# Kernel tuning notes

Measured on AMD Instinct MI355X. Metric: run time of the kernel, lower is better.

## Reference

```python
import jax, jax.numpy as jnp
import numpy as np

D_IN, H, V = 512, 1024, 32000
S, B, T = 64, 128, 48
MARGIN = 0.1


def setup_inputs() -> dict:
    key = jax.random.key(0)
    ks = jax.random.split(key, 16)
    sc = 0.05
    f = lambda k, shp: jax.random.normal(k, shp, jnp.float32) * sc
    emb_W = f(ks[0], (V, D_IN)).at[0].set(0.0)  # padding_idx=0 row is zero
    return dict(
        ctx=jax.random.normal(ks[1], (S, B, H), jnp.float32),
        ctx_mask=jnp.ones((S, B), jnp.float32),
        y=jax.random.randint(ks[2], (T, B), 0, V),
        emb_W=emb_W,
        W_init=f(ks[3], (H, H)), b_init=jnp.zeros((H,), jnp.float32),
        W_ih0=f(ks[4], (3 * H, D_IN)), W_hh0=f(ks[5], (3 * H, H)),
        b_ih0=jnp.zeros((3 * H,), jnp.float32), b_hh0=jnp.zeros((3 * H,), jnp.float32),
        W_c2c=f(ks[6], (H, H)), W_h2c=f(ks[7], (H, H)), v_att=f(ks[8], (H,)),
        W_ih1=f(ks[9], (3 * H, H)), W_hh1=f(ks[10], (3 * H, H)),
        b_ih1=jnp.zeros((3 * H,), jnp.float32), b_hh1=jnp.zeros((3 * H,), jnp.float32),
        W_h2o=f(ks[11], (D_IN, H)), b_h2o=jnp.zeros((D_IN,), jnp.float32),
        W_out=f(ks[12], (V, D_IN)),
    )


def _gru(x, h, Wih, Whh, bih, bhh):
    # torch.nn.GRUCell math
    gi = x @ Wih.T + bih
    gh = h @ Whh.T + bhh
    ir, iz, inn = jnp.split(gi, 3, axis=-1)
    hr, hz, hn = jnp.split(gh, 3, axis=-1)
    r = jax.nn.sigmoid(ir + hr)
    z = jax.nn.sigmoid(iz + hz)
    n = jnp.tanh(inn + r * hn)
    return (1.0 - z) * n + z * h


def reference(ctx, ctx_mask, y, emb_W, W_init, b_init, W_ih0, W_hh0, b_ih0, b_hh0,
              W_c2c, W_h2c, v_att, W_ih1, W_hh1, b_ih1, b_hh1, W_h2o, b_h2o, W_out):
    # dec_init='mean_ctx': tanh(FF(masked mean over source))
    mean_ctx = ctx.sum(0) / ctx_mask.sum(0)[:, None]            # (B,H)
    h = jnp.tanh(mean_ctx @ W_init.T + b_init)                  # h0 (B,H)

    ctx_p = jnp.einsum('sbc,dc->sbd', ctx, W_c2c)               # ctx2ctx, hoisted out of loop
    neg = jnp.where(ctx_mask > 0, 0.0, -1e9)                    # (S,B) additive mask
    W_out_n = W_out / jnp.linalg.norm(W_out, axis=-1, keepdims=True)

    emb_in = emb_W[y[:-1]]                                      # (T-1,B,D_IN)
    targets = y[1:]                                             # (T-1,B)

    def step(h, inp):
        e, tgt = inp
        h1 = _gru(e, h, W_ih0, W_hh0, b_ih0, b_hh0)             # dec0
        # MLP attention: v^T tanh(ctx2ctx(ctx) + hid2ctx(h1))
        scores = jnp.tanh(ctx_p + (h1 @ W_h2c.T)[None]) @ v_att + neg   # (S,B)
        alpha = jax.nn.softmax(scores, axis=0)
        z_t = jnp.einsum('sb,sbc->bc', alpha, ctx)              # context (B,H)
        h2 = _gru(z_t, h1, W_ih1, W_hh1, b_ih1, b_hh1)          # dec1
        logit = jnp.tanh(h2 @ W_h2o.T + b_h2o)                  # hid2out
        logit = logit / jnp.linalg.norm(logit, axis=-1, keepdims=True)
        log_p = logit @ W_out_n.T                               # (B,V) cosine sims
        # max-margin loss, contrastive_type='max', ignore pad (tgt==0)
        s_true = jnp.take_along_axis(log_p, tgt[:, None], axis=1)
        viol = jnp.maximum(MARGIN - s_true + log_p, 0.0)
        viol = viol * (1.0 - jax.nn.one_hot(tgt, V, dtype=log_p.dtype))
        l = jnp.sum(jnp.where(tgt != 0, viol.max(-1), 0.0))
        return h2, l

    _, losses = jax.lax.scan(step, h, (emb_in, targets))
    return losses.sum()
```

## Files before the change

### kernel.cpp

```cpp
#include <hip/hip_runtime.h>
#include <math.h>

#define H    1024
#define H3   3072
#define DIN  512
#define VSZ  32000
#define SS   64
#define BB   128
#define TP   47
#define NROWS (TP*BB)
#define VCHUNKS 250
#define FMARGIN 0.1f
#define NBLK 256
#define HS   65536
#define CTXPL_S 62

typedef unsigned short u16;
typedef unsigned int u32;
typedef unsigned long long u64;
typedef __bf16 bf16_t;
typedef bf16_t bf16x8 __attribute__((ext_vector_type(8)));
typedef float f32x4 __attribute__((ext_vector_type(4)));
typedef u16 u16x4 __attribute__((ext_vector_type(4)));
typedef u16 u16x8 __attribute__((ext_vector_type(8)));

#define MFMA __builtin_amdgcn_mfma_f32_16x16x32_bf16

__device__ inline u16 f2bf(float f){
    unsigned b = __float_as_uint(f);
    return (u16)((b + 0x7FFFu + ((b >> 16) & 1u)) >> 16);
}
__device__ inline float bf2f(u16 u){ return __uint_as_float(((unsigned)u) << 16); }
__device__ inline float sigm(float x){ return 1.f/(1.f + expf(-x)); }

__device__ inline void stoval(float* p, float v){ *p = v; }
__device__ inline void stoval(u16* p, float v){ *p = f2bf(v); }

__device__ inline void cstore(u32* p, u32 v){ __hip_atomic_store(p, v, __ATOMIC_RELAXED, __HIP_MEMORY_SCOPE_AGENT); }
__device__ inline void cstoref(float* p, float v){ __hip_atomic_store(p, v, __ATOMIC_RELAXED, __HIP_MEMORY_SCOPE_AGENT); }
__device__ inline void cstore64(u64* p, u64 v){ __hip_atomic_store(p, v, __ATOMIC_RELAXED, __HIP_MEMORY_SCOPE_AGENT); }
__device__ inline float cloadf(const float* p){ return __hip_atomic_load(p, __ATOMIC_RELAXED, __HIP_MEMORY_SCOPE_AGENT); }

__device__ inline void gbar(u32* bar, u32* mygen, int tid, int bid){
    __syncthreads();
    if (tid == 0){
        u32 tgt = ++(*mygen);
        __builtin_amdgcn_s_waitcnt(0);
        u32* cnt = bar + 64 + (bid >> 3)*32;
        u32 old = __hip_atomic_fetch_add(cnt, 1u, __ATOMIC_RELAXED, __HIP_MEMORY_SCOPE_AGENT);
        if (old == 7u){
            __hip_atomic_store(cnt, 0u, __ATOMIC_RELAXED, __HIP_MEMORY_SCOPE_AGENT);
            u32 old2 = __hip_atomic_fetch_add(&bar[1], 1u, __ATOMIC_RELEASE, __HIP_MEMORY_SCOPE_AGENT);
            if (old2 == 31u){
                __hip_atomic_store(&bar[1], 0u, __ATOMIC_RELAXED, __HIP_MEMORY_SCOPE_AGENT);
                __hip_atomic_store(&bar[0], tgt, __ATOMIC_RELEASE, __HIP_MEMORY_SCOPE_AGENT);
            }
        }
        while (__hip_atomic_load(&bar[0], __ATOMIC_RELAXED, __HIP_MEMORY_SCOPE_AGENT) < tgt)
            __builtin_amdgcn_s_sleep(1);
    }
    __syncthreads();
    asm volatile("" ::: "memory");
}


__global__ __launch_bounds__(128) void k_mask_sum(const float* __restrict__ mask, float* __restrict__ msum){
    int b = threadIdx.x;
    if (b < BB){ float s = 0.f; for (int i = 0; i < SS; i++) s += mask[i*BB + b]; msum[b] = s; }
}

__global__ __launch_bounds__(256) void k_mean_ctx(const float* __restrict__ ctx, const float* __restrict__ msum,
                                                  float* __restrict__ mean){
    int idx = blockIdx.x*256 + threadIdx.x;
    if (idx < BB*H){
        float s = 0.f;
        for (int i = 0; i < SS; i++) s += ctx[(size_t)i*BB*H + idx];
        mean[idx] = s / msum[idx / H];
    }
}

__global__ __launch_bounds__(256) void k_f32bf(const float* __restrict__ in, u16* __restrict__ out, int n4){
    int i = blockIdx.x*256 + threadIdx.x;
    if (i >= n4) return;
    float4 v = ((const float4*)in)[i];
    u16x4 o = { f2bf(v.x), f2bf(v.y), f2bf(v.z), f2bf(v.w) };
    ((u16x4*)out)[i] = o;
}

__global__ __launch_bounds__(256) void k_pack_h0(const float* __restrict__ h0, u32* __restrict__ hsHI,
                                                 u32* __restrict__ hsLO){
    int i = blockIdx.x*256 + threadIdx.x;
    float v0 = h0[i*2], v1 = h0[i*2 + 1];
    u16 a = f2bf(v0), b = f2bf(v1);
    hsHI[i] = (u32)a | ((u32)b << 16);
    hsLO[i] = (u32)f2bf(v0 - bf2f(a)) | ((u32)f2bf(v1 - bf2f(b)) << 16);
}

__global__ __launch_bounds__(256) void k_f2bf_frag(const float* __restrict__ in, u16* __restrict__ out,
                                                   int RK8, int K8){
    int t = blockIdx.x*256 + threadIdx.x;
    if (t >= RK8) return;
    int r = t / K8, k8 = t - r*K8;
    const float* p = in + (size_t)r*K8*8 + k8*8;
    float4 a = *(const float4*)p;
    float4 b = *(const float4*)(p + 4);
    size_t dst = ((size_t)(r >> 4)*(K8 >> 2) + (k8 >> 2))*512 + (size_t)((r & 15) + (k8 & 3)*16)*8;
    u16x8 o;
    o[0]=f2bf(a.x); o[1]=f2bf(a.y); o[2]=f2bf(a.z); o[3]=f2bf(a.w);
    o[4]=f2bf(b.x); o[5]=f2bf(b.y); o[6]=f2bf(b.z); o[7]=f2bf(b.w);
    *(u16x8*)(out + dst) = o;
}

__global__ __launch_bounds__(256) void k_rownorm_frag(const float* __restrict__ in, u16* __restrict__ out,
                                                      int nrows){
    int w = threadIdx.x >> 6, lane = threadIdx.x & 63;
    int row = blockIdx.x*4 + w;
    if (row >= nrows) return;
    const float* r = in + (size_t)row*512 + lane*8;
    float4 a = *(const float4*)r;
    float4 b = *(const float4*)(r + 4);
    float s = a.x*a.x + a.y*a.y + a.z*a.z + a.w*a.w
            + b.x*b.x + b.y*b.y + b.z*b.z + b.w*b.w;
    #pragma unroll
    for (int off = 32; off; off >>= 1) s += __shfl_xor(s, off);
    float inv = rsqrtf(s);
    size_t dst = ((size_t)(row >> 4)*16 + (lane >> 2))*512 + (size_t)((row & 15) + (lane & 3)*16)*8;
    u16x8 o;
    o[0]=f2bf(a.x*inv); o[1]=f2bf(a.y*inv); o[2]=f2bf(a.z*inv); o[3]=f2bf(a.w*inv);
    o[4]=f2bf(b.x*inv); o[5]=f2bf(b.y*inv); o[6]=f2bf(b.z*inv); o[7]=f2bf(b.w*inv);
    *(u16x8*)(out + dst) = o;
}

__global__ __launch_bounds__(256) void k_emb_frag(const float* __restrict__ emb, const int* __restrict__ y,
                                                  u16* __restrict__ out){
    int w = threadIdx.x >> 6, lane = threadIdx.x & 63;
    int row = blockIdx.x*4 + w;
    int src = y[row];
    const float* r = emb + (size_t)src*512 + lane*8;
    float4 a = *(const float4*)r;
    float4 b = *(const float4*)(r + 4);
    size_t dst = ((size_t)(row >> 4)*16 + (lane >> 2))*512 + (size_t)((row & 15) + (lane & 3)*16)*8;
    u16x8 o;
    o[0]=f2bf(a.x); o[1]=f2bf(a.y); o[2]=f2bf(a.z); o[3]=f2bf(a.w);
    o[4]=f2bf(b.x); o[5]=f2bf(b.y); o[6]=f2bf(b.z); o[7]=f2bf(b.w);
    *(u16x8*)(out + dst) = o;
}

template<int ACT>
__global__ __launch_bounds__(256) void k_gemm_nt(const float* __restrict__ A, const float* __restrict__ W,
                                                 const float* __restrict__ bias, float* __restrict__ C,
                                                 int M, int N, int K){
    __shared__ float As[16][68];
    __shared__ float Ws[16][68];
    int tid = threadIdx.x;
    int bm = blockIdx.y*64, bn = blockIdx.x*64;
    int lr = tid >> 2;
    int lk = (tid & 3) * 4;
    int tr = (tid >> 4) * 4;
    int tc = (tid & 15) * 4;
    float acc[4][4] = {};
    const float* Abase = A + (size_t)(bm + lr)*K;
    const float* Wbase = W + (size_t)(bn + lr)*K;
    for (int k0 = 0; k0 < K; k0 += 16){
        float4 av = *(const float4*)(Abase + k0 + lk);
        float4 wv = *(const float4*)(Wbase + k0 + lk);
        __syncthreads();
        As[lk+0][lr]=av.x; As[lk+1][lr]=av.y; As[lk+2][lr]=av.z; As[lk+3][lr]=av.w;
        Ws[lk+0][lr]=wv.x; Ws[lk+1][lr]=wv.y; Ws[lk+2][lr]=wv.z; Ws[lk+3][lr]=wv.w;
        __syncthreads();
        #pragma unroll
        for (int kk = 0; kk < 16; kk++){
            float4 a = *(const float4*)&As[kk][tr];
            float4 w = *(const float4*)&Ws[kk][tc];
            acc[0][0] += a.x*w.x; acc[0][1] += a.x*w.y; acc[0][2] += a.x*w.z; acc[0][3] += a.x*w.w;
            acc[1][0] += a.y*w.x; acc[1][1] += a.y*w.y; acc[1][2] += a.y*w.z; acc[1][3] += a.y*w.w;
            acc[2][0] += a.z*w.x; acc[2][1] += a.z*w.y; acc[2][2] += a.z*w.z; acc[2][3] += a.z*w.w;
            acc[3][0] += a.w*w.x; acc[3][1] += a.w*w.y; acc[3][2] += a.w*w.z; acc[3][3] += a.w*w.w;
        }
    }
    #pragma unroll
    for (int i = 0; i < 4; i++){
        #pragma unroll
        for (int j = 0; j < 4; j++){
            float v = acc[i][j];
            if (bias) v += bias[bn + tc + j];
            if (ACT == 1) v = tanhf(v);
            C[(size_t)(bm + tr + i)*N + bn + tc + j] = v;
        }
    }
}

template<int AFRAG, int ACT, typename OutT>
__global__ __launch_bounds__(256) void k_gemmf(const u16* __restrict__ A, const u16* __restrict__ B,
                                               const float* __restrict__ bias, OutT* __restrict__ C,
                                               int M, int N, int K){
    int tid = threadIdx.x, lane = tid & 63, w = tid >> 6;
    int wm = w >> 1, wn = w & 1;
    int row0 = blockIdx.y*128 + wm*64, col0 = blockIdx.x*128 + wn*64;
    int r16 = lane & 15, kg8 = (lane >> 4)*8, rg = (lane >> 4)*4;
    int K32 = K >> 5;
    f32x4 acc[4][4] = {};
    for (int k0 = 0; k0 < K32; k0++){
        bf16x8 af[4], bfv[4];
        #pragma unroll
        for (int i = 0; i < 4; i++){
            if (AFRAG) af[i] = *(const bf16x8*)(A + (((size_t)((row0 >> 4) + i)*K32 + k0) << 9) + lane*8);
            else       af[i] = *(const bf16x8*)(A + (size_t)(row0 + i*16 + r16)*K + k0*32 + kg8);
        }
        #pragma unroll
        for (int j = 0; j < 4; j++)
            bfv[j] = *(const bf16x8*)(B + (((size_t)((col0 >> 4) + j)*K32 + k0) << 9) + lane*8);
        #pragma unroll
        for (int i = 0; i < 4; i++)
            #pragma unroll
            for (int j = 0; j < 4; j++)
                acc[i][j] = MFMA(af[i], bfv[j], acc[i][j], 0, 0, 0);
    }
    #pragma unroll
    for (int i = 0; i < 4; i++){
        #pragma unroll
        for (int j = 0; j < 4; j++){
            #pragma unroll
            for (int r = 0; r < 4; r++){
                int row = row0 + i*16 + rg + r;
                int col = col0 + j*16 + r16;
                float v = acc[i][j][r];
                if (bias) v += bias[col];
                if (ACT) v = tanhf(v);
                stoval(C + (size_t)row*N + col, v);
            }
        }
    }
}

struct RI {
    const u16 *gi0, *Whh0, *Wh2c, *Wih1, *Whh1, *ctxp;
    const float *bhh0, *bih1, *bhh1, *vatt, *mask, *ctxf;
    u32 *hsHI, *hsLO, *h1HI, *h1LO, *ztHI, *ztLO;
    float *prF;
    float *ghF;
    float *spar;
    u16 *h2all;
    u32 *bar;
};

__global__ __launch_bounds__(512) void k_recur8(RI a){
    __shared__ u16 wlds[49152];
    __shared__ u16 ctxpL[CTXPL_S*512];
    __shared__ float sal[SS];
    const int tid = threadIdx.x, lane = tid & 63, wv = tid >> 6;
    const int bid = blockIdx.x;
    const int r16 = lane & 15, rg = (lane >> 4)*4, kq4 = (lane >> 4)*4;
    const int ab = (bid & 7)*16 + ((bid >> 3) >> 1);
    const int ahalf = (bid >> 3) & 1;
    u32 mygen = 0;

    {
        auto cp32k = [&](const u16* gsrc, int tile, int base){
            const u32* s = (const u32*)(gsrc + (size_t)tile*16384);
            u32* d = (u32*)(wlds + base);
            #pragma unroll
            for (int i = 0; i < 16; i++) d[tid + i*512] = s[tid + i*512];
        };
        if (bid < 64){
            cp32k(a.Whh0, bid, 0); cp32k(a.Whh0, 64+bid, 16384); cp32k(a.Whh0, 128+bid, 32768);
        } else if (bid < 128){
            int jt = bid - 64;
            cp32k(a.Wih1, jt, 0); cp32k(a.Wih1, 64+jt, 16384); cp32k(a.Wih1, 128+jt, 32768);
        } else if (bid < 192){
            int wt = bid - 128;
            cp32k(a.Whh1, 3*wt, 0); cp32k(a.Whh1, 3*wt+1, 16384); cp32k(a.Whh1, 3*wt+2, 32768);
        } else {
            cp32k(a.Wh2c, bid-192, 0);
        }
        for (int i = tid; i < CTXPL_S*512/8; i += 512){
            int s = (i*8) >> 9, h = (i*8) & 511;
            *(u16x8*)(ctxpL + i*8) = *(const u16x8*)(a.ctxp + ((size_t)(s*BB + ab))*H + ahalf*512 + h);
        }
    }
    float vv[8];
    {
        float4 v0 = *(const float4*)(a.vatt + ahalf*512 + lane*8);
        float4 v1 = *(const float4*)(a.vatt + ahalf*512 + lane*8 + 4);
        vv[0]=v0.x; vv[1]=v0.y; vv[2]=v0.z; vv[3]=v0.w;
        vv[4]=v1.x; vv[5]=v1.y; vv[6]=v1.z; vv[7]=v1.w;
    }
    __syncthreads();

    for (int t = 0; t < TP; t++){
        float* prT = a.prF + (size_t)t*BB*H;
        float* spT = a.spar + (size_t)t*256*SS;

        if (bid < 64){
            const u32* AbH = a.hsHI + (size_t)t*HS + (size_t)(wv*16 + r16)*512 + kq4;
            const u32* AbL = a.hsLO + (size_t)t*HS + (size_t)(wv*16 + r16)*512 + kq4;
            f32x4 ac0 = {}, ac1 = {}, ac2 = {};
            for (int k0 = 0; k0 < 32; k0++){
                bf16x8 ah = *(const bf16x8*)(AbH + k0*16);
                bf16x8 al = *(const bf16x8*)(AbL + k0*16);
                bf16x8 b0 = *(const bf16x8*)(wlds + (k0*64 + lane)*8);
                bf16x8 b1 = *(const bf16x8*)(wlds + 16384 + (k0*64 + lane)*8);
                bf16x8 b2 = *(const bf16x8*)(wlds + 32768 + (k0*64 + lane)*8);
                ac0 = MFMA(ah, b0, ac0, 0, 0, 0); ac0 = MFMA(al, b0, ac0, 0, 0, 0);
                ac1 = MFMA(ah, b1, ac1, 0, 0, 0); ac1 = MFMA(al, b1, ac1, 0, 0, 0);
                ac2 = MFMA(ah, b2, ac2, 0, 0, 0); ac2 = MFMA(al, b2, ac2, 0, 0, 0);
            }
            const u16* gi = a.gi0 + (size_t)t*BB*H3;
            const u32* hsH = a.hsHI + (size_t)t*HS;
            const u32* hsL = a.hsLO + (size_t)t*HS;
            int sh = (r16 & 1)*16;
            #pragma unroll
            for (int r = 0; r < 4; r++){
                int b = wv*16 + rg + r, j = bid*16 + r16;
                float gr = bf2f(gi[(size_t)b*H3 + j]);
                float gz = bf2f(gi[(size_t)b*H3 + H + j]);
                float gn = bf2f(gi[(size_t)b*H3 + 2*H + j]);
                float hr = ac0[r] + a.bhh0[j];
                float hz = ac1[r] + a.bhh0[H + j];
                float hn = ac2[r] + a.bhh0[2*H + j];
                u32 uh = hsH[(size_t)b*512 + (j >> 1)];
                u32 ul = hsL[(size_t)b*512 + (j >> 1)];
                float hp = bf2f((u16)(uh >> sh)) + bf2f((u16)(ul >> sh));
                float rr = sigm(gr + hr), zz = sigm(gz + hz);
                float nn = tanhf(gn + rr*hn);
                float hv = (1.f - zz)*nn + zz*hp;
                u16 hib = f2bf(hv);
                u16 lob = f2bf(hv - bf2f(hib));
                u32 hip = (u32)__shfl_xor((int)(u32)hib, 1);
                u32 lop = (u32)__shfl_xor((int)(u32)lob, 1);
                if (!(r16 & 1)){
                    cstore(a.h1HI + (size_t)t*HS + (size_t)b*512 + (j >> 1), (u32)hib | (hip << 16));
                    cstore(a.h1LO + (size_t)t*HS + (size_t)b*512 + (j >> 1), (u32)lob | (lop << 16));
                }
            }
        }
        gbar(a.bar, &mygen, tid, bid);

        if (bid >= 128){
            const u32* AbH = a.h1HI + (size_t)t*HS + (size_t)(wv*16 + r16)*512 + kq4;
            const u32* AbL = a.h1LO + (size_t)t*HS + (size_t)(wv*16 + r16)*512 + kq4;
            if (bid < 192){
                int wt = bid - 128;
                f32x4 ac0 = {}, ac1 = {}, ac2 = {};
                for (int k0 = 0; k0 < 32; k0++){
                    bf16x8 ah = *(const bf16x8*)(AbH + k0*16);
                    bf16x8 al = *(const bf16x8*)(AbL + k0*16);
                    bf16x8 b0 = *(const bf16x8*)(wlds + (k0*64 + lane)*8);
                    bf16x8 b1 = *(const bf16x8*)(wlds + 16384 + (k0*64 + lane)*8);
                    bf16x8 b2 = *(const bf16x8*)(wlds + 32768 + (k0*64 + lane)*8);
                    ac0 = MFMA(ah, b0, ac0, 0, 0, 0); ac0 = MFMA(al, b0, ac0, 0, 0, 0);
                    ac1 = MFMA(ah, b1, ac1, 0, 0, 0); ac1 = MFMA(al, b1, ac1, 0, 0, 0);
                    ac2 = MFMA(ah, b2, ac2, 0, 0, 0); ac2 = MFMA(al, b2, ac2, 0, 0, 0);
                }
                #pragma unroll
                for (int r = 0; r < 4; r++){
                    int b = wv*16 + rg + r;
                    int c0 = wt*48 + r16;
                    float p0 = __shfl_xor(ac0[r], 1);
                    float p1 = __shfl_xor(ac1[r], 1);
                    float p2 = __shfl_xor(ac2[r], 1);
                    if (!(r16 & 1)){
                        cstore64((u64*)(a.ghF + (size_t)b*H3 + c0),
                                 (u64)__float_as_uint(ac0[r]) | ((u64)__float_as_uint(p0) << 32));
                        cstore64((u64*)(a.ghF + (size_t)b*H3 + c0 + 16),
                                 (u64)__float_as_uint(ac1[r]) | ((u64)__float_as_uint(p1) << 32));
                        cstore64((u64*)(a.ghF + (size_t)b*H3 + c0 + 32),
                                 (u64)__float_as_uint(ac2[r]) | ((u64)__float_as_uint(p2) << 32));
                    }
                }
            } else {
                f32x4 ac = {};
                for (int k0 = 0; k0 < 32; k0++){
                    bf16x8 ah = *(const bf16x8*)(AbH + k0*16);
                    bf16x8 al = *(const bf16x8*)(AbL + k0*16);
                    bf16x8 bv = *(const bf16x8*)(wlds + (k0*64 + lane)*8);
                    ac = MFMA(ah, bv, ac, 0, 0, 0); ac = MFMA(al, bv, ac, 0, 0, 0);
                }
                #pragma unroll
                for (int r = 0; r < 4; r++){
                    int b = wv*16 + rg + r;
                    int c0 = (bid - 192)*16 + r16;
                    float p0 = __shfl_xor(ac[r], 1);
                    if (!(r16 & 1))
                        cstore64((u64*)(prT + (size_t)b*H + c0),
                                 (u64)__float_as_uint(ac[r]) | ((u64)__float_as_uint(p0) << 32));
                }
            }
        }
        gbar(a.bar, &mygen, tid, bid);

        {
            float pj[8];
            {
                float4 q0 = *(const float4*)(prT + (size_t)ab*H + ahalf*512 + lane*8);
                float4 q1 = *(const float4*)(prT + (size_t)ab*H + ahalf*512 + lane*8 + 4);
                pj[0]=q0.x; pj[1]=q0.y; pj[2]=q0.z; pj[3]=q0.w;
                pj[4]=q1.x; pj[5]=q1.y; pj[6]=q1.z; pj[7]=q1.w;
            }
            #pragma unroll
            for (int q = 0; q < 8; q++){
                int s = wv*8 + q;
                u16x8 cv;
                if (s < CTXPL_S) cv = *(const u16x8*)(ctxpL + s*512 + lane*8);
                else cv = *(const u16x8*)(a.ctxp + ((size_t)(s*BB + ab))*H + ahalf*512 + lane*8);
                float acc = 0.f;
                #pragma unroll
                for (int e = 0; e < 8; e++) acc += tanhf(bf2f(cv[e]) + pj[e]) * vv[e];
                #pragma unroll
                for (int off = 32; off; off >>= 1) acc += __shfl_xor(acc, off);
                if (lane == 0) cstoref(spT + (ab*2 + ahalf)*SS + s, acc);
            }
        }
        gbar(a.bar, &mygen, tid, bid);

        {
            if (tid < 64){
                float v = spT[(ab*2)*SS + tid] + spT[(ab*2 + 1)*SS + tid]
                        + ((a.mask[tid*BB + ab] > 0.f) ? 0.f : -1e9f);
                float m = v;
                #pragma unroll
                for (int off = 32; off; off >>= 1) m = fmaxf(m, __shfl_xor(m, off));
                float e = expf(v - m);
                float su = e;
                #pragma unroll
                for (int off = 32; off; off >>= 1) su += __shfl_xor(su, off);
                sal[tid] = e / su;
            }
            __syncthreads();
            int col = tid;
            const float* cbase = a.ctxf + (size_t)ab*H + ahalf*512 + col;
            float z = 0.f;
            #pragma unroll 8
            for (int s = 0; s < SS; s++)
                z += sal[s] * cbase[(size_t)s*BB*H];
            float zp = __shfl_xor(z, 1);
            if (!(tid & 1)){
                int j0 = ahalf*512 + col;
                u16 z0 = f2bf(z), z1 = f2bf(zp);
                cstore(a.ztHI + (size_t)t*HS + (size_t)ab*512 + (j0 >> 1), (u32)z0 | ((u32)z1 << 16));
                cstore(a.ztLO + (size_t)t*HS + (size_t)ab*512 + (j0 >> 1),
                       (u32)f2bf(z - bf2f(z0)) | ((u32)f2bf(zp - bf2f(z1)) << 16));
            }
            __syncthreads();
        }
        gbar(a.bar, &mygen, tid, bid);

        if (bid >= 64 && bid < 128){
            int jt = bid - 64;
            const u32* AbH = a.ztHI + (size_t)t*HS + (size_t)(wv*16 + r16)*512 + kq4;
            const u32* AbL = a.ztLO + (size_t)t*HS + (size_t)(wv*16 + r16)*512 + kq4;
            f32x4 ac0 = {}, ac1 = {}, ac2 = {};
            for (int k0 = 0; k0 < 32; k0++){
                bf16x8 ah = *(const bf16x8*)(AbH + k0*16);
                bf16x8 al = *(const bf16x8*)(AbL + k0*16);
                bf16x8 b0 = *(const bf16x8*)(wlds + (k0*64 + lane)*8);
                bf16x8 b1 = *(const bf16x8*)(wlds + 16384 + (k0*64 + lane)*8);
                bf16x8 b2 = *(const bf16x8*)(wlds + 32768 + (k0*64 + lane)*8);
                ac0 = MFMA(ah, b0, ac0, 0, 0, 0); ac0 = MFMA(al, b0, ac0, 0, 0, 0);
                ac1 = MFMA(ah, b1, ac1, 0, 0, 0); ac1 = MFMA(al, b1, ac1, 0, 0, 0);
                ac2 = MFMA(ah, b2, ac2, 0, 0, 0); ac2 = MFMA(al, b2, ac2, 0, 0, 0);
            }
            const u32* h1H = a.h1HI + (size_t)t*HS;
            const u32* h1L = a.h1LO + (size_t)t*HS;
            int sh = (r16 & 1)*16;
            #pragma unroll
            for (int r = 0; r < 4; r++){
                int b = wv*16 + rg + r, j = jt*16 + r16;
                float gr = ac0[r] + a.bih1[j];
                float gz = ac1[r] + a.bih1[H + j];
                float gn = ac2[r] + a.bih1[2*H + j];
                float hr = cloadf(a.ghF + (size_t)b*H3 + j)       + a.bhh1[j];
                float hz = cloadf(a.ghF + (size_t)b*H3 + H + j)   + a.bhh1[H + j];
                float hn = cloadf(a.ghF + (size_t)b*H3 + 2*H + j) + a.bhh1[2*H + j];
                u32 uh = h1H[(size_t)b*512 + (j >> 1)];
                u32 ul = h1L[(size_t)b*512 + (j >> 1)];
                float h1v = bf2f((u16)(uh >> sh)) + bf2f((u16)(ul >> sh));
                float rr = sigm(gr + hr), zz = sigm(gz + hz);
                float nn = tanhf(gn + rr*hn);
                float hv = (1.f - zz)*nn + zz*h1v;
                a.h2all[((size_t)t*BB + b)*H + j] = f2bf(hv);
                u16 hib = f2bf(hv);
                u16 lob = f2bf(hv - bf2f(hib));
                u32 hip = (u32)__shfl_xor((int)(u32)hib, 1);
                u32 lop = (u32)__shfl_xor((int)(u32)lob, 1);
                if (!(r16 & 1)){
                    cstore(a.hsHI + (size_t)(t+1)*HS + (size_t)b*512 + (j >> 1), (u32)hib | (hip << 16));
                    cstore(a.hsLO + (size_t)(t+1)*HS + (size_t)b*512 + (j >> 1), (u32)lob | (lop << 16));
                }
            }
        }
        gbar(a.bar, &mygen, tid, bid);
    }
}

__global__ __launch_bounds__(256) void k_final(const u16* __restrict__ logitf, const u16* __restrict__ Wf,
                                               const int* __restrict__ y, float* __restrict__ pmax,
                                               float* __restrict__ strue){
    __shared__ float red[128][2];
    int tid = threadIdx.x, w = tid >> 6, lane = tid & 63;
    int wm = w >> 1, wn = w & 1;
    int row0 = blockIdx.x*128 + wm*64;
    int col0 = blockIdx.y*128 + wn*64;
    int r16 = lane & 15, rg = (lane >> 4)*4;
    f32x4 acc[4][4] = {};
    for (int k0 = 0; k0 < 16; k0++){
        bf16x8 af[4], bfv[4];
        #pragma unroll
        for (int i = 0; i < 4; i++)
            af[i] = *(const bf16x8*)(logitf + (((size_t)((row0 >> 4) + i)*16 + k0) << 9) + lane*8);
        #pragma unroll
        for (int j = 0; j < 4; j++)
            bfv[j] = *(const bf16x8*)(Wf + (((size_t)((col0 >> 4) + j)*16 + k0) << 9) + lane*8);
        #pragma unroll
        for (int i = 0; i < 4; i++)
            #pragma unroll
            for (int j = 0; j < 4; j++)
                acc[i][j] = MFMA(af[i], bfv[j], acc[i][j], 0, 0, 0);
    }
    #pragma unroll
    for (int i = 0; i < 4; i++){
        #pragma unroll
        for (int r = 0; r < 4; r++){
            int row = row0 + i*16 + rg + r;
            int tgt = y[row + BB];
            float m = -1e30f;
            #pragma unroll
            for (int j = 0; j < 4; j++){
                float v = acc[i][j][r];
                int col = col0 + j*16 + r16;
                if (col == tgt){ strue[row] = v; v = -1e30f; }
                m = fmaxf(m, v);
            }
            m = fmaxf(m, __shfl_xor(m, 1));
            m = fmaxf(m, __shfl_xor(m, 2));
            m = fmaxf(m, __shfl_xor(m, 4));
            m = fmaxf(m, __shfl_xor(m, 8));
            if (r16 == 0) red[wm*64 + i*16 + rg + r][wn] = m;
        }
    }
    __syncthreads();
    if (tid < 128){
        float m = fmaxf(red[tid][0], red[tid][1]);
        pmax[(size_t)(blockIdx.x*128 + tid)*VCHUNKS + blockIdx.y] = m;
    }
}

__global__ __launch_bounds__(256) void k_loss(const float* __restrict__ pmax, const float* __restrict__ strue,
                                              const int* __restrict__ y, float* __restrict__ out){
    int R = blockIdx.x*256 + threadIdx.x;
    int lane = threadIdx.x & 63, wave = threadIdx.x >> 6;
    float l = 0.f;
    if (R < NROWS){
        int tgt = y[R + BB];
        if (tgt != 0){
            const float* pm = pmax + (size_t)R*VCHUNKS;
            float m = -1e30f;
            for (int i = 0; i < VCHUNKS; i++) m = fmaxf(m, pm[i]);
            l = fmaxf(FMARGIN - strue[R] + m, 0.f);
        }
    }
    #pragma unroll
    for (int off = 32; off; off >>= 1) l += __shfl_down(l, off);
    __shared__ float wsum[4];
    if (lane == 0) wsum[wave] = l;
    __syncthreads();
    if (threadIdx.x == 0) atomicAdd(out, wsum[0] + wsum[1] + wsum[2] + wsum[3]);
}

extern "C" void kernel_launch(void* const* d_in, const int* in_sizes, int n_in,
                              void* d_out, int out_size, void* d_ws, size_t ws_size,
                              hipStream_t stream){
    const float* ctx    = (const float*)d_in[0];
    const float* mask   = (const float*)d_in[1];
    const int*   y      = (const int*)d_in[2];
    const float* emb_W  = (const float*)d_in[3];
    const float* W_init = (const float*)d_in[4];
    const float* b_init = (const float*)d_in[5];
    const float* W_ih0  = (const float*)d_in[6];
    const float* W_hh0  = (const float*)d_in[7];
    const float* b_ih0  = (const float*)d_in[8];
    const float* b_hh0  = (const float*)d_in[9];
    const float* W_c2c  = (const float*)d_in[10];
    const float* W_h2c  = (const float*)d_in[11];
    const float* v_att  = (const float*)d_in[12];
    const float* W_ih1  = (const float*)d_in[13];
    const float* W_hh1  = (const float*)d_in[14];
    const float* b_ih1  = (const float*)d_in[15];
    const float* b_hh1  = (const float*)d_in[16];
    const float* W_h2o  = (const float*)d_in[17];
    const float* b_h2o  = (const float*)d_in[18];
    const float* W_out  = (const float*)d_in[19];
    float* out = (float*)d_out;

    char* wsb = (char*)d_ws;
    size_t off = 0;
    auto alloc = [&](size_t bytes)->void*{
        void* p = (void*)(wsb + off);
        off = (off + bytes + 255) & ~(size_t)255;
        return p;
    };
    u16* Wih0f = (u16*)alloc((size_t)H3*DIN*2);
    u16* Whh0f = (u16*)alloc((size_t)H3*H*2);
    u16* Wih1f = (u16*)alloc((size_t)H3*H*2);
    u16* Whh1f = (u16*)alloc((size_t)H3*H*2);
    u16* Wh2cf = (u16*)alloc((size_t)H*H*2);
    u16* Wc2cf = (u16*)alloc((size_t)H*H*2);
    u16* Wh2of = (u16*)alloc((size_t)DIN*H*2);
    u16* Woutf = (u16*)alloc((size_t)VSZ*DIN*2);
    u16* ctxb  = (u16*)alloc((size_t)SS*BB*H*2);
    u16* ctxpb = (u16*)alloc((size_t)SS*BB*H*2);
    u16* embf  = (u16*)alloc((size_t)NROWS*DIN*2);
    u16* gi0b  = (u16*)alloc((size_t)NROWS*H3*2);
    u16* h2allb= (u16*)alloc((size_t)NROWS*H*2);
    u32* hsHI  = (u32*)alloc((size_t)(TP+1)*HS*4);
    u32* hsLO  = (u32*)alloc((size_t)(TP+1)*HS*4);
    u32* h1HI  = (u32*)alloc((size_t)TP*HS*4);
    u32* h1LO  = (u32*)alloc((size_t)TP*HS*4);
    u32* ztHI  = (u32*)alloc((size_t)TP*HS*4);
    u32* ztLO  = (u32*)alloc((size_t)TP*HS*4);
    float* ghF = (float*)alloc((size_t)BB*H3*4);
    float* spar= (float*)alloc((size_t)TP*256*SS*4);
    u32* bar   = (u32*)alloc(8192);
    float* strue  = (float*)alloc(NROWS*4);
    float* msum   = (float*)alloc(BB*4);
    float* meanc  = (float*)alloc((size_t)BB*H*4);
    float* h0f    = (float*)alloc((size_t)BB*H*4);

    float* prF = (float*)Woutf;

    float* logitf  = (float*)gi0b;
    u16*   logitfr = (u16*)(gi0b + (size_t)NROWS*DIN*2);
    float* pmax    = (float*)(gi0b + (size_t)NROWS*DIN*2 + (size_t)NROWS*DIN);

    hipMemsetAsync(d_out, 0, sizeof(float), stream);
    hipMemsetAsync(bar, 0, 8192, stream);

    hipLaunchKernelGGL(k_mask_sum, dim3(1), dim3(128), 0, stream, mask, msum);
    hipLaunchKernelGGL(k_mean_ctx, dim3(BB*H/256), dim3(256), 0, stream, ctx, msum, meanc);
    hipLaunchKernelGGL((k_gemm_nt<1>), dim3(H/64, BB/64), dim3(256), 0, stream,
                       meanc, W_init, b_init, h0f, BB, H, H);
    hipLaunchKernelGGL(k_pack_h0, dim3(HS/256), dim3(256), 0, stream, h0f, hsHI, hsLO);

    hipLaunchKernelGGL(k_f2bf_frag, dim3(H3*DIN/8/256), dim3(256), 0, stream, W_ih0, Wih0f, H3*DIN/8, DIN/8);
    hipLaunchKernelGGL(k_f2bf_frag, dim3(H3*H/8/256), dim3(256), 0, stream, W_hh0, Whh0f, H3*H/8, H/8);
    hipLaunchKernelGGL(k_f2bf_frag, dim3(H3*H/8/256), dim3(256), 0, stream, W_ih1, Wih1f, H3*H/8, H/8);
    hipLaunchKernelGGL(k_f2bf_frag, dim3(H3*H/8/256), dim3(256), 0, stream, W_hh1, Whh1f, H3*H/8, H/8);
    hipLaunchKernelGGL(k_f2bf_frag, dim3(H*H/8/256), dim3(256), 0, stream, W_h2c, Wh2cf, H*H/8, H/8);
    hipLaunchKernelGGL(k_f2bf_frag, dim3(H*H/8/256), dim3(256), 0, stream, W_c2c, Wc2cf, H*H/8, H/8);
    hipLaunchKernelGGL(k_f2bf_frag, dim3(DIN*H/8/256), dim3(256), 0, stream, W_h2o, Wh2of, DIN*H/8, H/8);
    hipLaunchKernelGGL(k_f32bf, dim3(SS*BB*H/4/256), dim3(256), 0, stream, ctx, ctxb, SS*BB*H/4);
    hipLaunchKernelGGL(k_emb_frag, dim3(NROWS/4), dim3(256), 0, stream, emb_W, y, embf);

    hipLaunchKernelGGL((k_gemmf<1,0,u16>), dim3(H3/128, NROWS/128), dim3(256), 0, stream,
                       embf, Wih0f, b_ih0, gi0b, NROWS, H3, DIN);
    hipLaunchKernelGGL((k_gemmf<0,0,u16>), dim3(H/128, SS*BB/128), dim3(256), 0, stream,
                       ctxb, Wc2cf, (const float*)nullptr, ctxpb, SS*BB, H, H);

    RI ri;
    ri.gi0 = gi0b; ri.Whh0 = Whh0f; ri.Wh2c = Wh2cf; ri.Wih1 = Wih1f; ri.Whh1 = Whh1f;
    ri.ctxp = ctxpb;
    ri.bhh0 = b_hh0; ri.bih1 = b_ih1; ri.bhh1 = b_hh1; ri.vatt = v_att; ri.mask = mask; ri.ctxf = ctx;
    ri.hsHI = hsHI; ri.hsLO = hsLO; ri.h1HI = h1HI; ri.h1LO = h1LO; ri.ztHI = ztHI; ri.ztLO = ztLO;
    ri.prF = prF; ri.ghF = ghF; ri.spar = spar;
    ri.h2all = h2allb; ri.bar = bar;
    void* kp[] = { (void*)&ri };
    hipLaunchCooperativeKernel((const void*)k_recur8, dim3(NBLK), dim3(512), kp, 0, stream);

    hipLaunchKernelGGL(k_rownorm_frag, dim3(VSZ/4), dim3(256), 0, stream, W_out, Woutf, VSZ);
    hipLaunchKernelGGL((k_gemmf<0,1,float>), dim3(DIN/128, NROWS/128), dim3(256), 0, stream,
                       h2allb, Wh2of, b_h2o, logitf, NROWS, DIN, H);
    hipLaunchKernelGGL(k_rownorm_frag, dim3(NROWS/4), dim3(256), 0, stream, logitf, logitfr, NROWS);
    hipLaunchKernelGGL(k_final, dim3(NROWS/128, VSZ/128), dim3(256), 0, stream,
                       logitfr, Woutf, y, pmax, strue);
    hipLaunchKernelGGL(k_loss, dim3((NROWS + 255)/256), dim3(256), 0, stream, pmax, strue, y, out);
}
```

Before: 5.126 ms.

## Replace attention grid barrier with pairwise flags and spread barrier release words

Inside the persistent recurrent kernel, the grid-wide barrier between the attention-score partials and the softmax is replaced by a pairwise flag handshake between the two blocks that share a batch element. Each block now waits only for its partner's half of the scores. The global barrier release is also written to eight separate cache-line-spaced words, so spinning blocks poll different addresses instead of one hot word, and the spin sleep is lengthened. This removes one full grid synchronisation per timestep and reduces polling contention, at the cost of extra flag memory and more fragile ordering logic.

```diff
diff --git a/kernel.cpp b/kernel.cpp
--- a/kernel.cpp
+++ b/kernel.cpp
@@ -53,11 +53,14 @@
             u32 old2 = __hip_atomic_fetch_add(&bar[1], 1u, __ATOMIC_RELEASE, __HIP_MEMORY_SCOPE_AGENT);
             if (old2 == 31u){
                 __hip_atomic_store(&bar[1], 0u, __ATOMIC_RELAXED, __HIP_MEMORY_SCOPE_AGENT);
-                __hip_atomic_store(&bar[0], tgt, __ATOMIC_RELEASE, __HIP_MEMORY_SCOPE_AGENT);
-            }
-        }
-        while (__hip_atomic_load(&bar[0], __ATOMIC_RELAXED, __HIP_MEMORY_SCOPE_AGENT) < tgt)
-            __builtin_amdgcn_s_sleep(1);
+                #pragma unroll
+                for (int x = 0; x < 8; x++)
+                    __hip_atomic_store(&bar[1536 + x*32], tgt, __ATOMIC_RELEASE, __HIP_MEMORY_SCOPE_AGENT);
+            }
+        }
+        u32* rel = &bar[1536 + (bid & 7)*32];
+        while (__hip_atomic_load(rel, __ATOMIC_RELAXED, __HIP_MEMORY_SCOPE_AGENT) < tgt)
+            __builtin_amdgcn_s_sleep(2);
     }
     __syncthreads();
     asm volatile("" ::: "memory");
@@ -233,18 +236,19 @@
     }
 }
 
-struct RI {
+struct RJ {
     const u16 *gi0, *Whh0, *Wh2c, *Wih1, *Whh1, *ctxp;
     const float *bhh0, *bih1, *bhh1, *vatt, *mask, *ctxf;
     u32 *hsHI, *hsLO, *h1HI, *h1LO, *ztHI, *ztLO;
     float *prF;
     float *ghF;
     float *spar;
+    u32 *flg;
     u16 *h2all;
     u32 *bar;
 };
 
-__global__ __launch_bounds__(512) void k_recur8(RI a){
+__global__ __launch_bounds__(512) void k_recur9(RJ a){
     __shared__ u16 wlds[49152];
     __shared__ u16 ctxpL[CTXPL_S*512];
     __shared__ float sal[SS];
@@ -410,12 +414,16 @@
                 for (int off = 32; off; off >>= 1) acc += __shfl_xor(acc, off);
                 if (lane == 0) cstoref(spT + (ab*2 + ahalf)*SS + s, acc);
             }
-        }
-        gbar(a.bar, &mygen, tid, bid);
-
-        {
+            __syncthreads();
+            if (tid == 0){
+                __builtin_amdgcn_s_waitcnt(0);
+                __hip_atomic_store(&a.flg[(ab*2 + ahalf)*32], (u32)(t+1), __ATOMIC_RELEASE, __HIP_MEMORY_SCOPE_AGENT);
+                while (__hip_atomic_load(&a.flg[(ab*2 + (1-ahalf))*32], __ATOMIC_ACQUIRE, __HIP_MEMORY_SCOPE_AGENT) < (u32)(t+1))
+                    __builtin_amdgcn_s_sleep(1);
+            }
+            __syncthreads();
             if (tid < 64){
-                float v = spT[(ab*2)*SS + tid] + spT[(ab*2 + 1)*SS + tid]
+                float v = cloadf(spT + (ab*2)*SS + tid) + cloadf(spT + (ab*2 + 1)*SS + tid)
                         + ((a.mask[tid*BB + ab] > 0.f) ? 0.f : -1e9f);
                 float m = v;
                 #pragma unroll
@@ -621,6 +629,7 @@
     float* ghF = (float*)alloc((size_t)BB*H3*4);
     float* spar= (float*)alloc((size_t)TP*256*SS*4);
     u32* bar   = (u32*)alloc(8192);
+    u32* flg   = (u32*)alloc(32768);
     float* strue  = (float*)alloc(NROWS*4);
     float* msum   = (float*)alloc(BB*4);
     float* meanc  = (float*)alloc((size_t)BB*H*4);
@@ -634,6 +643,7 @@
 
     hipMemsetAsync(d_out, 0, sizeof(float), stream);
     hipMemsetAsync(bar, 0, 8192, stream);
+    hipMemsetAsync(flg, 0, 32768, stream);
 
     hipLaunchKernelGGL(k_mask_sum, dim3(1), dim3(128), 0, stream, mask, msum);
     hipLaunchKernelGGL(k_mean_ctx, dim3(BB*H/256), dim3(256), 0, stream, ctx, msum, meanc);
@@ -656,15 +666,15 @@
     hipLaunchKernelGGL((k_gemmf<0,0,u16>), dim3(H/128, SS*BB/128), dim3(256), 0, stream,
                        ctxb, Wc2cf, (const float*)nullptr, ctxpb, SS*BB, H, H);
 
-    RI ri;
-    ri.gi0 = gi0b; ri.Whh0 = Whh0f; ri.Wh2c = Wh2cf; ri.Wih1 = Wih1f; ri.Whh1 = Whh1f;
-    ri.ctxp = ctxpb;
-    ri.bhh0 = b_hh0; ri.bih1 = b_ih1; ri.bhh1 = b_hh1; ri.vatt = v_att; ri.mask = mask; ri.ctxf = ctx;
-    ri.hsHI = hsHI; ri.hsLO = hsLO; ri.h1HI = h1HI; ri.h1LO = h1LO; ri.ztHI = ztHI; ri.ztLO = ztLO;
-    ri.prF = prF; ri.ghF = ghF; ri.spar = spar;
-    ri.h2all = h2allb; ri.bar = bar;
-    void* kp[] = { (void*)&ri };
-    hipLaunchCooperativeKernel((const void*)k_recur8, dim3(NBLK), dim3(512), kp, 0, stream);
+    RJ rj;
+    rj.gi0 = gi0b; rj.Whh0 = Whh0f; rj.Wh2c = Wh2cf; rj.Wih1 = Wih1f; rj.Whh1 = Whh1f;
+    rj.ctxp = ctxpb;
+    rj.bhh0 = b_hh0; rj.bih1 = b_ih1; rj.bhh1 = b_hh1; rj.vatt = v_att; rj.mask = mask; rj.ctxf = ctx;
+    rj.hsHI = hsHI; rj.hsLO = hsLO; rj.h1HI = h1HI; rj.h1LO = h1LO; rj.ztHI = ztHI; rj.ztLO = ztLO;
+    rj.prF = prF; rj.ghF = ghF; rj.spar = spar; rj.flg = flg;
+    rj.h2all = h2allb; rj.bar = bar;
+    void* kp[] = { (void*)&rj };
+    hipLaunchCooperativeKernel((const void*)k_recur9, dim3(NBLK), dim3(512), kp, 0, stream);
 
     hipLaunchKernelGGL(k_rownorm_frag, dim3(VSZ/4), dim3(256), 0, stream, W_out, Woutf, VSZ);
     hipLaunchKernelGGL((k_gemmf<0,1,float>), dim3(DIN/128, NROWS/128), dim3(256), 0, stream,
```

Result: faster. 4.785 ms (median of 2 runs) (-6.7%).
